# Kernel tuning notes

Measured on AMD Instinct MI355X. Metric: run time of the kernel, lower is better.

## Reference

```python
import jax, jax.numpy as jnp
import numpy as np

EPS = 1.1920929e-07  # torch RMSNorm default eps = finfo(fp32).eps
NUM_HEADS = 8
UP_HEAD = 64
ROPE_HEAD = 32
TOP_K = 4
HIDDEN = 512
INTER = 256
DQ = 256
DKV = 128
N_EXPERTS = 16
B, S = 2, 2048


def _rmsnorm(x, w):
    return x * jax.lax.rsqrt(jnp.mean(x * x, axis=-1, keepdims=True) + EPS) * w


def _rope(x):
    # x: [B, h, S, D] with D = ROPE_HEAD; rotate-half RoPE, base 10000
    D = x.shape[-1]
    s = x.shape[-2]
    inv_freq = 1.0 / (10000.0 ** (jnp.arange(0, D, 2, dtype=jnp.float32) / D))
    freqs = jnp.outer(jnp.arange(s, dtype=jnp.float32), inv_freq)  # [S, D/2]
    emb = jnp.concatenate([freqs, freqs], axis=-1)  # [S, D]
    cos, sin = jnp.cos(emb), jnp.sin(emb)
    x1, x2 = x[..., : D // 2], x[..., D // 2:]
    rot = jnp.concatenate([-x2, x1], axis=-1)
    return x * cos + rot * sin


def _swiglu(x, wg, wu, wd):
    return (jax.nn.silu(x @ wg) * (x @ wu)) @ wd


def setup_inputs() -> dict:
    key = jax.random.key(0)
    ks = jax.random.split(key, 18)
    sd = 0.02
    inp = {
        "hidden_states": jax.random.normal(ks[0], (B, S, HIDDEN), jnp.float32),
        "w_in_norm": jnp.ones((HIDDEN,), jnp.float32),
        "w_dq": sd * jax.random.normal(ks[1], (HIDDEN, DQ), jnp.float32),
        "w_qnorm": jnp.ones((DQ,), jnp.float32),
        "w_uq": sd * jax.random.normal(ks[2], (DQ, NUM_HEADS * (UP_HEAD + ROPE_HEAD)), jnp.float32),
        "w_dkv": sd * jax.random.normal(ks[3], (HIDDEN, DKV + ROPE_HEAD), jnp.float32),
        "w_kvnorm": jnp.ones((DKV,), jnp.float32),
        "w_ukv": sd * jax.random.normal(ks[4], (DKV, NUM_HEADS * UP_HEAD * 2), jnp.float32),
        "w_o": sd * jax.random.normal(ks[5], (NUM_HEADS * UP_HEAD, HIDDEN), jnp.float32),
        "w_post_norm": jnp.ones((HIDDEN,), jnp.float32),
        "w_gate": sd * jax.random.normal(ks[6], (HIDDEN, N_EXPERTS), jnp.float32),
        "sh_wg": sd * jax.random.normal(ks[7], (HIDDEN, INTER), jnp.float32),
        "sh_wu": sd * jax.random.normal(ks[8], (HIDDEN, INTER), jnp.float32),
        "sh_wd": sd * jax.random.normal(ks[9], (INTER, HIDDEN), jnp.float32),
        "r_wg": sd * jax.random.normal(ks[10], (N_EXPERTS, HIDDEN, INTER), jnp.float32),
        "r_wu": sd * jax.random.normal(ks[11], (N_EXPERTS, HIDDEN, INTER), jnp.float32),
        "r_wd": sd * jax.random.normal(ks[12], (N_EXPERTS, INTER, HIDDEN), jnp.float32),
    }
    return inp


def reference(hidden_states, w_in_norm, w_dq, w_qnorm, w_uq, w_dkv, w_kvnorm,
              w_ukv, w_o, w_post_norm, w_gate, sh_wg, sh_wu, sh_wd,
              r_wg, r_wu, r_wd):
    b, s, h = hidden_states.shape
    # ---- MLA attention block ----
    residual = hidden_states
    x = _rmsnorm(hidden_states, w_in_norm)
    c_q = x @ w_dq                                             # [B,S,Dq]
    qcr = _rmsnorm(c_q, w_qnorm) @ w_uq                        # [B,S,nh*(uh+rh)]
    qcr = qcr.reshape(b, s, NUM_HEADS, UP_HEAD + ROPE_HEAD).transpose(0, 2, 1, 3)
    q_c, q_r = qcr[..., :UP_HEAD], qcr[..., UP_HEAD:]
    ckv_kr = x @ w_dkv                                         # [B,S,Dkv+rh]
    c_kv, k_r = ckv_kr[..., :DKV], ckv_kr[..., DKV:]
    k_r = k_r[:, None, :, :]                                   # [B,1,S,rh]
    kv = (_rmsnorm(c_kv, w_kvnorm) @ w_ukv).reshape(b, s, NUM_HEADS, 2 * UP_HEAD).transpose(0, 2, 1, 3)
    k_c, v = kv[..., :UP_HEAD], kv[..., UP_HEAD:]
    q = jnp.concatenate([q_c, _rope(q_r)], axis=-1)            # [B,nh,S,96]
    k = jnp.concatenate([k_c, jnp.broadcast_to(_rope(k_r), (b, NUM_HEADS, s, ROPE_HEAD))], axis=-1)
    scale = 1.0 / jnp.sqrt(jnp.float32(UP_HEAD + ROPE_HEAD))
    attn = jax.nn.softmax(jnp.einsum('bhqd,bhkd->bhqk', q, k) * scale, axis=-1)
    o = jnp.einsum('bhqk,bhkd->bhqd', attn, v).transpose(0, 2, 1, 3).reshape(b, s, NUM_HEADS * UP_HEAD)
    x = o @ w_o + residual
    # ---- MoE block ----
    residual = x
    x = _rmsnorm(x, w_post_norm)
    x2 = x.reshape(-1, h)                                      # [T,H]
    shared = _swiglu(x2, sh_wg, sh_wu, sh_wd)                  # [T,H]
    scores = jax.nn.sigmoid(x2 @ w_gate)                       # [T,E]
    tw, ti = jax.lax.top_k(scores, TOP_K)                      # [T,k]
    tw = tw / jnp.sum(tw, axis=-1, keepdims=True)
    # combine[t,e] = routing weight of expert e for token t (0 if not selected)
    combine = jnp.sum(jax.nn.one_hot(ti, N_EXPERTS, dtype=x2.dtype) * tw[..., None], axis=1)  # [T,E]
    g = jnp.einsum('th,ehi->tei', x2, r_wg)
    u = jnp.einsum('th,ehi->tei', x2, r_wu)
    y = jnp.einsum('tei,eih->teh', jax.nn.silu(g) * u, r_wd)   # per-expert SwiGLU outputs
    routed = jnp.einsum('teh,te->th', y, combine)
    return (shared + routed).reshape(b, s, h) + residual
```

## Files before the change

### kernel.cpp

```cpp
#include <hip/hip_runtime.h>
#include <hip/hip_bf16.h>
#include <math.h>

typedef float f32x4 __attribute__((ext_vector_type(4)));
typedef short s16x8 __attribute__((ext_vector_type(8)));

constexpr int Tt = 4096;
constexpr int NEn = 16;
constexpr float EPSf = 1.1920929e-07f;

__device__ __forceinline__ short f2b(float f) {
    union { __hip_bfloat16 h; short s; } u;
    u.h = __float2bfloat16(f);
    return u.s;
}
__device__ __forceinline__ float b2f(short s) {
    union { float f; unsigned u; } v;
    v.u = ((unsigned)(unsigned short)s) << 16;
    return v.f;
}

constexpr size_t alg(size_t x) { return (x + 15) & ~(size_t)15; }
constexpr size_t OFF_CQKV = 0;
constexpr size_t OFF_QCR  = alg(OFF_CQKV + (size_t)Tt * 416);
constexpr size_t OFF_KVB  = alg(OFF_QCR  + (size_t)Tt * 768);
constexpr size_t OFF_R2   = alg(OFF_KVB  + (size_t)Tt * 1024);
constexpr size_t OFF_TOKE = alg(OFF_R2   + (size_t)Tt * 512);
constexpr size_t OFF_TOKW = alg(OFF_TOKE + (size_t)Tt * 4);
constexpr size_t OFF_EWT  = alg(OFF_TOKW + (size_t)Tt * 4);
constexpr size_t OFF_ECNT = alg(OFF_EWT  + (size_t)NEn * Tt);
constexpr size_t OFF_ETOK = alg(OFF_ECNT + 64);
constexpr size_t OFF_WL   = alg(OFF_ETOK + (size_t)NEn * Tt);
constexpr size_t OFF_WCNT = alg(OFF_WL   + 160);
constexpr size_t OFF_PO   = 0;
constexpr size_t OFF_PL   = (size_t)16 * 2048 * 4 * 64 / 2;
constexpr size_t OFF_XNB   = alg(OFF_WCNT + 16);
constexpr size_t OFF_CQNB  = alg(OFF_XNB   + (size_t)Tt * 512 / 2);
constexpr size_t OFF_CKVNB = alg(OFF_CQNB  + (size_t)Tt * 256 / 2);
constexpr size_t OFF_QB    = alg(OFF_CKVNB + (size_t)Tt * 128 / 2);
constexpr size_t OFF_KB    = alg(OFF_QB    + (size_t)16 * 2048 * 96 / 2);
constexpr size_t OFF_VBT   = alg(OFF_KB    + (size_t)16 * 2048 * 96 / 2);
constexpr size_t OFF_AOB   = alg(OFF_VBT   + (size_t)16 * 64 * 2048 / 2);
constexpr size_t OFF_XN2B  = alg(OFF_AOB   + (size_t)Tt * 512 / 2);
constexpr size_t OFF_GACT  = alg(OFF_XN2B  + (size_t)Tt * 512 / 2);
constexpr size_t OFF_EACT  = alg(OFF_GACT  + (size_t)Tt * 256 / 2);
constexpr size_t OFF_WQKVT = alg(OFF_EACT  + (size_t)16384 * 256 / 2);
constexpr size_t OFF_WUQT  = alg(OFF_WQKVT + (size_t)416 * 512 / 2);
constexpr size_t OFF_WUKVT = alg(OFF_WUQT  + (size_t)768 * 256 / 2);
constexpr size_t OFF_WOT   = alg(OFF_WUKVT + (size_t)1024 * 128 / 2);
constexpr size_t OFF_SHWGT = alg(OFF_WOT   + (size_t)512 * 512 / 2);
constexpr size_t OFF_SHWUT = alg(OFF_SHWGT + (size_t)256 * 512 / 2);
constexpr size_t OFF_SHWDT = alg(OFF_SHWUT + (size_t)256 * 512 / 2);
constexpr size_t OFF_RWGT  = alg(OFF_SHWDT + (size_t)512 * 256 / 2);
constexpr size_t OFF_RWUT  = alg(OFF_RWGT  + (size_t)16 * 256 * 512 / 2);
constexpr size_t OFF_RWDT  = alg(OFF_RWUT  + (size_t)16 * 256 * 512 / 2);

struct CvtTab {
    const float* src[11];
    short* dst[11];
    int K[11], N[11], end[11];
};
__global__ __launch_bounds__(256)
void k_cvt_all(CvtTab tab) {
    __shared__ float t[32][33];
    int bid = blockIdx.x;
    int i = 0;
    while (bid >= tab.end[i]) ++i;
    int tloc = bid - (i ? tab.end[i - 1] : 0);
    int K = tab.K[i], N = tab.N[i];
    int ntiles = N >> 5, perE = ntiles * (K >> 5);
    int e = tloc / perE, rem = tloc - e * perE;
    int k0 = (rem / ntiles) << 5, n0 = (rem % ntiles) << 5;
    size_t eo = (size_t)e * K * N;
    const float* src = tab.src[i];
    short* dst = tab.dst[i];
    int c = threadIdx.x & 31, r = threadIdx.x >> 5;
#pragma unroll
    for (int q = 0; q < 4; ++q)
        t[r + 8 * q][c] = src[eo + (size_t)(k0 + r + 8 * q) * N + n0 + c];
    __syncthreads();
#pragma unroll
    for (int q = 0; q < 4; ++q)
        dst[eo + (size_t)(n0 + r + 8 * q) * K + k0 + c] = f2b(t[c][r + 8 * q]);
}

__global__ void k_rms(const float* __restrict__ in, int inStride, const float* __restrict__ w,
                      short* __restrict__ outB, int outStride, int D) {
    int row = blockIdx.x, tid = threadIdx.x;
    __shared__ float xs[512];
    __shared__ float red[256];
    const float* ip = in + (size_t)row * inStride;
    float ss = 0.f;
    for (int i = tid; i < D; i += 256) { float v = ip[i]; xs[i] = v; ss += v * v; }
    red[tid] = ss; __syncthreads();
    for (int s = 128; s > 0; s >>= 1) { if (tid < s) red[tid] += red[tid + s]; __syncthreads(); }
    float sc = rsqrtf(red[0] / (float)D + EPSf);
    for (int i = tid; i < D; i += 256) outB[(size_t)row * outStride + i] = f2b(xs[i] * sc * w[i]);
}

__global__ void k_rms2(const float* __restrict__ cqkv, const float* __restrict__ wq, short* __restrict__ cqnb,
                       const float* __restrict__ wkv, short* __restrict__ ckvnb) {
    int row = blockIdx.x, tid = threadIdx.x;
    __shared__ float xs[256];
    __shared__ float red[256];
    const float* ip; const float* w; short* ob; int D, outStride, r;
    if (row < Tt) { r = row;      ip = cqkv + (size_t)r * 416;       w = wq;  ob = cqnb;  D = 256; outStride = 256; }
    else          { r = row - Tt; ip = cqkv + (size_t)r * 416 + 256; w = wkv; ob = ckvnb; D = 128; outStride = 128; }
    float ss = 0.f;
    for (int i = tid; i < D; i += 256) { float v = ip[i]; xs[i] = v; ss += v * v; }
    red[tid] = ss; __syncthreads();
    for (int s = 128; s > 0; s >>= 1) { if (tid < s) red[tid] += red[tid + s]; __syncthreads(); }
    float sc = rsqrtf(red[0] / (float)D + EPSf);
    for (int i = tid; i < D; i += 256) ob[(size_t)r * outStride + i] = f2b(xs[i] * sc * w[i]);
}

__global__ __launch_bounds__(256)
void k_rms_router(const float* __restrict__ r2, const float* __restrict__ wpost,
                  const float* __restrict__ wg,
                  short* __restrict__ xn2b, int4* __restrict__ toke, float4* __restrict__ tokw) {
    int t = blockIdx.x, tid = threadIdx.x;
    __shared__ float xs[512];
    __shared__ float red[256];
    __shared__ float part[16][17];
    __shared__ float sc[16];
    const float* ip = r2 + (size_t)t * 512;
    float ss = 0.f;
    for (int i = tid; i < 512; i += 256) { float v = ip[i]; xs[i] = v; ss += v * v; }
    red[tid] = ss; __syncthreads();
    for (int s = 128; s > 0; s >>= 1) { if (tid < s) red[tid] += red[tid + s]; __syncthreads(); }
    float scale = rsqrtf(red[0] / 512.f + EPSf);
    for (int i = tid; i < 512; i += 256) {
        float v = xs[i] * scale * wpost[i];
        xs[i] = v;
        xn2b[(size_t)t * 512 + i] = f2b(v);
    }
    __syncthreads();
    {
        int e = tid & 15, ch = tid >> 4;
        const float* wp = wg + (size_t)ch * 32 * 16 + e;
        float s = 0.f;
#pragma unroll 8
        for (int k = 0; k < 32; ++k) s = fmaf(xs[ch * 32 + k], wp[(size_t)k * 16], s);
        part[ch][e] = s;
    }
    __syncthreads();
    if (tid < 16) {
        float s = 0.f;
#pragma unroll
        for (int c = 0; c < 16; ++c) s += part[c][tid];
        sc[tid] = 1.f / (1.f + expf(-s));
    }
    __syncthreads();
    if (tid < 64) {
        int lane = tid, e = lane & 15;
        float scv = sc[e];
        unsigned sel = 0;
        float tw[4]; int ti[4];
#pragma unroll
        for (int kk = 0; kk < 4; ++kk) {
            float cand = ((sel >> e) & 1u) ? -1e30f : scv;
            float mx = cand;
            mx = fmaxf(mx, __shfl_xor(mx, 1));
            mx = fmaxf(mx, __shfl_xor(mx, 2));
            mx = fmaxf(mx, __shfl_xor(mx, 4));
            mx = fmaxf(mx, __shfl_xor(mx, 8));
            unsigned long long msk = __ballot(cand == mx);
            int bi = (__ffsll(msk) - 1) & 15;
            tw[kk] = mx; ti[kk] = bi;
            sel |= 1u << bi;
        }
        if (lane == 0) {
            float inv = 1.f / (tw[0] + tw[1] + tw[2] + tw[3]);
            toke[t] = make_int4(ti[0], ti[1], ti[2], ti[3]);
            tokw[t] = make_float4(tw[0] * inv, tw[1] * inv, tw[2] * inv, tw[3] * inv);
        }
    }
}

template <int EPI>
__global__ __launch_bounds__(512)
void k_mgemm(const short* __restrict__ A, const short* __restrict__ BT,
             float* __restrict__ C, const float* __restrict__ add, int N, int K) {
    __shared__ __align__(16) short As[64 * 64];
    __shared__ __align__(16) short Bs[64 * 64];
    int tid = threadIdx.x;
    int w = tid >> 6, l = tid & 63, g = l >> 4, li = l & 15;
    int wm = w >> 1, wn = w & 1;
    int m0 = blockIdx.y * 64, n0 = blockIdx.x * 64;
    f32x4 acc[2] = {};
    for (int k0 = 0; k0 < K; k0 += 64) {
        __syncthreads();
        {
            int row = tid >> 3, ch = tid & 7;
            *(int4*)&As[row * 64 + ((ch ^ (row & 7)) * 8)] =
                *(const int4*)(A + (size_t)(m0 + row) * K + k0 + 8 * ch);
            int4 v = {0, 0, 0, 0};
            if (n0 + row < N) v = *(const int4*)(BT + (size_t)(n0 + row) * K + k0 + 8 * ch);
            *(int4*)&Bs[row * 64 + ((ch ^ (row & 7)) * 8)] = v;
        }
        __syncthreads();
#pragma unroll
        for (int kc = 0; kc < 2; ++kc) {
            int row = wm * 16 + li;
            s16x8 af = *(const s16x8*)&As[row * 64 + (((4 * kc + g) ^ (li & 7)) * 8)];
#pragma unroll
            for (int nt = 0; nt < 2; ++nt) {
                int n = wn * 32 + nt * 16 + li;
                s16x8 bf = *(const s16x8*)&Bs[n * 64 + (((4 * kc + g) ^ (li & 7)) * 8)];
                acc[nt] = __builtin_amdgcn_mfma_f32_16x16x32_bf16(af, bf, acc[nt], 0, 0, 0);
            }
        }
    }
#pragma unroll
    for (int nt = 0; nt < 2; ++nt)
#pragma unroll
        for (int r = 0; r < 4; ++r) {
            int gm = m0 + wm * 16 + 4 * g + r;
            int gn = n0 + wn * 32 + nt * 16 + li;
            if (gn < N) {
                float v = acc[nt][r];
                if (EPI == 1) v += add[(size_t)gm * N + gn];
                C[(size_t)gm * N + gn] = v;
            }
        }
}

__global__ __launch_bounds__(512)
void k_shexp(const short* __restrict__ X, const short* __restrict__ WGt, const short* __restrict__ WUt,
             short* __restrict__ gact) {
    __shared__ __align__(16) short As[64 * 64];
    __shared__ __align__(16) short Bg[64 * 64];
    __shared__ __align__(16) short Bu[64 * 64];
    int tid = threadIdx.x;
    int w = tid >> 6, l = tid & 63, g = l >> 4, li = l & 15;
    int wm = w >> 1, wn = w & 1;
    int m0 = blockIdx.x * 64, n0 = blockIdx.y * 64;
    f32x4 ag[2] = {}, au[2] = {};
    for (int k0 = 0; k0 < 512; k0 += 64) {
        __syncthreads();
        {
            int row = tid >> 3, ch = tid & 7;
            *(int4*)&As[row * 64 + ((ch ^ (row & 7)) * 8)] =
                *(const int4*)(X + (size_t)(m0 + row) * 512 + k0 + 8 * ch);
            *(int4*)&Bg[row * 64 + ((ch ^ (row & 7)) * 8)] =
                *(const int4*)(WGt + (size_t)(n0 + row) * 512 + k0 + 8 * ch);
            *(int4*)&Bu[row * 64 + ((ch ^ (row & 7)) * 8)] =
                *(const int4*)(WUt + (size_t)(n0 + row) * 512 + k0 + 8 * ch);
        }
        __syncthreads();
#pragma unroll
        for (int kc = 0; kc < 2; ++kc) {
            int row = wm * 16 + li;
            s16x8 af = *(const s16x8*)&As[row * 64 + (((4 * kc + g) ^ (li & 7)) * 8)];
#pragma unroll
            for (int nt = 0; nt < 2; ++nt) {
                int n = wn * 32 + nt * 16 + li;
                s16x8 bg = *(const s16x8*)&Bg[n * 64 + (((4 * kc + g) ^ (li & 7)) * 8)];
                s16x8 bu = *(const s16x8*)&Bu[n * 64 + (((4 * kc + g) ^ (li & 7)) * 8)];
                ag[nt] = __builtin_amdgcn_mfma_f32_16x16x32_bf16(af, bg, ag[nt], 0, 0, 0);
                au[nt] = __builtin_amdgcn_mfma_f32_16x16x32_bf16(af, bu, au[nt], 0, 0, 0);
            }
        }
    }
#pragma unroll
    for (int nt = 0; nt < 2; ++nt)
#pragma unroll
        for (int r = 0; r < 4; ++r) {
            int gm = m0 + wm * 16 + 4 * g + r;
            int gn = n0 + wn * 32 + nt * 16 + li;
            float gv = ag[nt][r], uv = au[nt][r];
            gact[(size_t)gm * 256 + gn] = f2b(gv / (1.f + __expf(-gv)) * uv);
        }
}

__global__ void k_build_qkv(const float* __restrict__ qcr, const float* __restrict__ kvb,
                            const float* __restrict__ cqkv,
                            short* __restrict__ qb, short* __restrict__ kb, short* __restrict__ vbt) {
    const float scale = 0.14724389f;
    int gid = blockIdx.x * 256 + threadIdx.x;
    const int NQ = 16 * 2048 * 96;
    if (gid < NQ) {
        int d = gid % 96;
        int rs = gid / 96;
        int srow = rs & 2047;
        int bh = rs >> 11;
        int b = bh >> 3, h = bh & 7;
        int t = b * 2048 + srow;
        const float* src = qcr + (size_t)t * 768 + h * 96;
        float val;
        if (d < 64) {
            val = src[d];
        } else {
            int d2 = d - 64;
            int fi = d2 & 15;
            float ang = (float)srow * __expf(-((float)(2 * fi) / 32.f) * 9.210340371976184f);
            float s, c; __sincosf(ang, &s, &c);
            float x = src[64 + d2];
            float r = (d2 < 16) ? -src[64 + d2 + 16] : src[64 + d2 - 16];
            val = x * c + r * s;
        }
        qb[gid] = f2b(val * scale);
    } else if (gid < 2 * NQ) {
        int g2 = gid - NQ;
        int d = g2 % 96;
        int rs = g2 / 96;
        int srow = rs & 2047;
        int bh = rs >> 11;
        int b = bh >> 3, h = bh & 7;
        int t = b * 2048 + srow;
        float val;
        if (d < 64) {
            val = kvb[(size_t)t * 1024 + h * 128 + d];
        } else {
            int d2 = d - 64;
            int fi = d2 & 15;
            float ang = (float)srow * __expf(-((float)(2 * fi) / 32.f) * 9.210340371976184f);
            float s, c; __sincosf(ang, &s, &c);
            float x = cqkv[(size_t)t * 416 + 384 + d2];
            float r = (d2 < 16) ? -cqkv[(size_t)t * 416 + 384 + d2 + 16]
                                :  cqkv[(size_t)t * 416 + 384 + d2 - 16];
            val = x * c + r * s;
        }
        kb[g2] = f2b(val);
    } else {
        int g2 = gid - 2 * NQ;
        int key = g2 & 2047;
        int dim = (g2 >> 11) & 63;
        int bh = g2 >> 17;
        int b = bh >> 3, h = bh & 7;
        vbt[g2] = f2b(kvb[(size_t)(b * 2048 + key) * 1024 + h * 128 + 64 + dim]);
    }
}

__global__ __launch_bounds__(256)
void k_attn(const short* __restrict__ qb, const short* __restrict__ kb,
            const short* __restrict__ vbt, short* __restrict__ po, float* __restrict__ pl) {
    __shared__ __align__(16) short Ks[64 * 100];
    __shared__ __align__(16) short Vs[80 * 64];
    int tid = threadIdx.x;
    int w = tid >> 6, l = tid & 63, g = l >> 4, li = l & 15;
    int blk = blockIdx.x;
    int bh = blk >> 6, rem = blk & 63;
    int qt = rem >> 2, ks = rem & 3;
    int qc0 = qt * 128 + w * 32;

    {
        const short one = 0x3F80;
        for (int i = tid; i < 16 * 64; i += 256)
            Vs[64 * 64 + i] = (i < 64) ? one : (short)0;
    }

    s16x8 qf[2][3];
#pragma unroll
    for (int j = 0; j < 2; ++j) {
        const short* qp = qb + (size_t)(bh * 2048 + qc0 + j * 16 + li) * 96;
#pragma unroll
        for (int c = 0; c < 3; ++c) qf[j][c] = *(const s16x8*)(qp + 32 * c + 8 * g);
    }

    f32x4 o[2][5] = {};
    const short* kbase = kb + (size_t)bh * 2048 * 96;
    const short* vbase = vbt + (size_t)bh * 64 * 2048;

    for (int t = 0; t < 8; ++t) {
        int koff = ks * 512 + t * 64;
        __syncthreads();
#pragma unroll
        for (int p = 0; p < 3; ++p) {
            int flat = p * 256 + tid;
            int key = flat / 12, u = flat % 12;
            *(int4*)&Ks[key * 100 + 8 * u] = *(const int4*)(kbase + (size_t)(koff + key) * 96 + 8 * u);
        }
#pragma unroll
        for (int p = 0; p < 2; ++p) {
            int flat = p * 256 + tid;
            int dim = flat >> 3, kc8 = flat & 7;
            int4 v = *(const int4*)(vbase + (size_t)dim * 2048 + koff + 8 * kc8);
            int sw = dim & 15;
            *(int2*)&Vs[dim * 64 + (((2 * kc8) ^ sw) * 4)]     = make_int2(v.x, v.y);
            *(int2*)&Vs[dim * 64 + (((2 * kc8 + 1) ^ sw) * 4)] = make_int2(v.z, v.w);
        }
        __syncthreads();

        f32x4 s[2][4];
#pragma unroll
        for (int kt = 0; kt < 4; ++kt) {
            f32x4 a0 = {}, a1 = {};
#pragma unroll
            for (int c = 0; c < 3; ++c) {
                s16x8 kf = *(const s16x8*)&Ks[(kt * 16 + li) * 100 + 32 * c + 8 * g];
                a0 = __builtin_amdgcn_mfma_f32_16x16x32_bf16(kf, qf[0][c], a0, 0, 0, 0);
                a1 = __builtin_amdgcn_mfma_f32_16x16x32_bf16(kf, qf[1][c], a1, 0, 0, 0);
            }
            s[0][kt] = a0; s[1][kt] = a1;
        }
#pragma unroll
        for (int j = 0; j < 2; ++j)
#pragma unroll
            for (int kt = 0; kt < 4; ++kt)
#pragma unroll
                for (int r = 0; r < 4; ++r) s[j][kt][r] = exp2f(s[j][kt][r]);
        s16x8 pf[2][2];
#pragma unroll
        for (int j = 0; j < 2; ++j)
#pragma unroll
            for (int kc = 0; kc < 2; ++kc) {
                s16x8 tt;
#pragma unroll
                for (int r = 0; r < 4; ++r) { tt[r] = f2b(s[j][2 * kc][r]); tt[4 + r] = f2b(s[j][2 * kc + 1][r]); }
                pf[j][kc] = tt;
            }
#pragma unroll
        for (int dt = 0; dt < 5; ++dt) {
            int dim = dt * 16 + li;
#pragma unroll
            for (int kc = 0; kc < 2; ++kc) {
                int2 a0 = *(const int2*)&Vs[dim * 64 + (((8 * kc + g) ^ li) * 4)];
                int2 a1 = *(const int2*)&Vs[dim * 64 + (((8 * kc + 4 + g) ^ li) * 4)];
                union { s16x8 v; int i[4]; } vf;
                vf.i[0] = a0.x; vf.i[1] = a0.y; vf.i[2] = a1.x; vf.i[3] = a1.y;
                o[0][dt] = __builtin_amdgcn_mfma_f32_16x16x32_bf16(vf.v, pf[0][kc], o[0][dt], 0, 0, 0);
                o[1][dt] = __builtin_amdgcn_mfma_f32_16x16x32_bf16(vf.v, pf[1][kc], o[1][dt], 0, 0, 0);
            }
        }
    }
#pragma unroll
    for (int j = 0; j < 2; ++j) {
        int qcol = qc0 + j * 16 + li;
        size_t qbase = ((size_t)(bh * 2048 + qcol) * 4 + ks) * 64;
#pragma unroll
        for (int dt = 0; dt < 4; ++dt)
#pragma unroll
            for (int r = 0; r < 4; ++r)
                po[qbase + dt * 16 + 4 * g + r] = f2b(o[j][dt][r]);
        if (g == 0) pl[(size_t)(bh * 2048 + qcol) * 4 + ks] = o[j][4][0];
    }
}

__global__ __launch_bounds__(256)
void k_attn_comb(const short* __restrict__ po, const float* __restrict__ pl, short* __restrict__ ao) {
    int gid = blockIdx.x * 256 + threadIdx.x;
    int d = gid & 63;
    int q = (gid >> 6) & 2047;
    int bh = gid >> 17;
    int b = bh >> 3, h = bh & 7;
    size_t pb = ((size_t)(bh * 2048 + q) * 4) * 64 + d;
    float os = 0.f;
#pragma unroll
    for (int ks = 0; ks < 4; ++ks) os += b2f(po[pb + 64 * ks]);
    size_t lb = (size_t)(bh * 2048 + q) * 4;
    float ls = pl[lb] + pl[lb + 1] + pl[lb + 2] + pl[lb + 3];
    ao[(size_t)(b * 2048 + q) * 512 + h * 64 + d] = f2b(os / ls);
}

__global__ __launch_bounds__(256)
void k_scatter(const int4* __restrict__ toke, const float4* __restrict__ tokw,
               float* __restrict__ ewt, int* __restrict__ ecnt, int* __restrict__ etok) {
    __shared__ int lcnt[16];
    __shared__ int lbase[16];
    int tid = threadIdx.x;
    int t = blockIdx.x * 256 + tid;
    if (tid < 16) lcnt[tid] = 0;
    __syncthreads();
    int4 e4 = toke[t];
    float4 w4 = tokw[t];
    int es[4] = { e4.x, e4.y, e4.z, e4.w };
    float wv[4] = { w4.x, w4.y, w4.z, w4.w };
    int ls[4];
#pragma unroll
    for (int kk = 0; kk < 4; ++kk) ls[kk] = atomicAdd(&lcnt[es[kk]], 1);
    __syncthreads();
    if (tid < 16) lbase[tid] = atomicAdd(&ecnt[tid], lcnt[tid]);
    __syncthreads();
#pragma unroll
    for (int kk = 0; kk < 4; ++kk) {
        int slot = lbase[es[kk]] + ls[kk];
        etok[es[kk] * 4096 + slot] = t * 4 + kk;
        ewt[es[kk] * 4096 + slot] = wv[kk];
    }
}

__global__ void k_worklist(const int* __restrict__ ecnt, int* __restrict__ wl, int* __restrict__ wcnt) {
    if (threadIdx.x == 0 && blockIdx.x == 0) {
        int c = 0;
        for (int e = 0; e < 16; ++e) {
            int n = (ecnt[e] + 127) >> 7;
            for (int i = 0; i < n; ++i) wl[c++] = (e << 20) | (i << 7);
        }
        wcnt[0] = c;
    }
}

__global__ __launch_bounds__(512)
void k_moe1m(const short* __restrict__ X, const short* __restrict__ WGt, const short* __restrict__ WUt,
             const int* __restrict__ ecnt, const int* __restrict__ etok,
             const int* __restrict__ wl, const int* __restrict__ wcnt,
             short* __restrict__ eact) {
    if ((int)blockIdx.x >= wcnt[0]) return;
    int ent = wl[blockIdx.x];
    int e = ent >> 20, base = ent & 0xFFFFF;
    int rows = min(128, ecnt[e] - base);
    int n0 = blockIdx.y * 64;
    __shared__ __align__(16) short As[128 * 64];
    __shared__ __align__(16) short Bg[64 * 64];
    __shared__ __align__(16) short Bu[64 * 64];
    __shared__ int toks[128];
    int tid = threadIdx.x;
    if (tid < 128) toks[tid] = (tid < rows) ? etok[e * 4096 + base + tid] : -1;
    __syncthreads();
    int w = tid >> 6, l = tid & 63, g = l >> 4, li = l & 15;
    int wm = w >> 1, wn = w & 1;
    const short* wgp = WGt + (size_t)e * 256 * 512;
    const short* wup = WUt + (size_t)e * 256 * 512;
    f32x4 ag[2][2] = {}, au[2][2] = {};
    for (int k0 = 0; k0 < 512; k0 += 64) {
        __syncthreads();
#pragma unroll
        for (int p = 0; p < 2; ++p) {
            int flat = p * 512 + tid;
            int row = flat >> 3, ch = flat & 7;
            int tk = toks[row];
            int4 v = {0, 0, 0, 0};
            if (tk >= 0) v = *(const int4*)(X + (size_t)(tk >> 2) * 512 + k0 + 8 * ch);
            *(int4*)&As[row * 64 + ((ch ^ (row & 7)) * 8)] = v;
        }
        {
            int n = tid >> 3, ch = tid & 7;
            *(int4*)&Bg[n * 64 + ((ch ^ (n & 7)) * 8)] = *(const int4*)(wgp + (size_t)(n0 + n) * 512 + k0 + 8 * ch);
            *(int4*)&Bu[n * 64 + ((ch ^ (n & 7)) * 8)] = *(const int4*)(wup + (size_t)(n0 + n) * 512 + k0 + 8 * ch);
        }
        __syncthreads();
#pragma unroll
        for (int kc = 0; kc < 2; ++kc) {
            s16x8 af[2], bg[2], bu[2];
#pragma unroll
            for (int mt = 0; mt < 2; ++mt) {
                int row = wm * 32 + mt * 16 + li;
                af[mt] = *(const s16x8*)&As[row * 64 + (((4 * kc + g) ^ (li & 7)) * 8)];
            }
#pragma unroll
            for (int nt = 0; nt < 2; ++nt) {
                int n = wn * 32 + nt * 16 + li;
                bg[nt] = *(const s16x8*)&Bg[n * 64 + (((4 * kc + g) ^ (li & 7)) * 8)];
                bu[nt] = *(const s16x8*)&Bu[n * 64 + (((4 * kc + g) ^ (li & 7)) * 8)];
            }
#pragma unroll
            for (int mt = 0; mt < 2; ++mt)
#pragma unroll
                for (int nt = 0; nt < 2; ++nt) {
                    ag[mt][nt] = __builtin_amdgcn_mfma_f32_16x16x32_bf16(af[mt], bg[nt], ag[mt][nt], 0, 0, 0);
                    au[mt][nt] = __builtin_amdgcn_mfma_f32_16x16x32_bf16(af[mt], bu[nt], au[mt][nt], 0, 0, 0);
                }
        }
    }
#pragma unroll
    for (int mt = 0; mt < 2; ++mt)
#pragma unroll
        for (int nt = 0; nt < 2; ++nt)
#pragma unroll
            for (int r = 0; r < 4; ++r) {
                int local = wm * 32 + mt * 16 + 4 * g + r;
                if (local < rows) {
                    int entry = toks[local];
                    int gn = n0 + wn * 32 + nt * 16 + li;
                    float gv = ag[mt][nt][r], uv = au[mt][nt][r];
                    eact[(size_t)entry * 256 + gn] = f2b(gv / (1.f + __expf(-gv)) * uv);
                }
            }
}

__global__ __launch_bounds__(512)
void k_moe2m(const short* __restrict__ EA, const short* __restrict__ WDt,
             const int* __restrict__ ecnt, const int* __restrict__ etok,
             const int* __restrict__ wl, const int* __restrict__ wcnt,
             const float* __restrict__ ewt, float* __restrict__ oacc) {
    if ((int)blockIdx.x >= wcnt[0]) return;
    int ent = wl[blockIdx.x];
    int e = ent >> 20, base = ent & 0xFFFFF;
    int rows = min(128, ecnt[e] - base);
    int n0 = blockIdx.y * 64;
    __shared__ __align__(16) short As[128 * 64];
    __shared__ __align__(16) short Bs[64 * 64];
    __shared__ int toks[128];
    __shared__ float wts[128];
    int tid = threadIdx.x;
    if (tid < 128) {
        toks[tid] = (tid < rows) ? etok[e * 4096 + base + tid] : -1;
        wts[tid]  = (tid < rows) ? ewt[e * 4096 + base + tid] : 0.f;
    }
    __syncthreads();
    int w = tid >> 6, l = tid & 63, g = l >> 4, li = l & 15;
    int wm = w >> 1, wn = w & 1;
    const short* wdp = WDt + (size_t)e * 512 * 256;
    f32x4 acc[2][2] = {};
    for (int k0 = 0; k0 < 256; k0 += 64) {
        __syncthreads();
#pragma unroll
        for (int p = 0; p < 2; ++p) {
            int flat = p * 512 + tid;
            int row = flat >> 3, ch = flat & 7;
            int tk = toks[row];
            int4 v = {0, 0, 0, 0};
            if (tk >= 0) v = *(const int4*)(EA + (size_t)tk * 256 + k0 + 8 * ch);
            *(int4*)&As[row * 64 + ((ch ^ (row & 7)) * 8)] = v;
        }
        {
            int n = tid >> 3, ch = tid & 7;
            *(int4*)&Bs[n * 64 + ((ch ^ (n & 7)) * 8)] = *(const int4*)(wdp + (size_t)(n0 + n) * 256 + k0 + 8 * ch);
        }
        __syncthreads();
#pragma unroll
        for (int kc = 0; kc < 2; ++kc) {
            s16x8 af[2], bf[2];
#pragma unroll
            for (int mt = 0; mt < 2; ++mt) {
                int row = wm * 32 + mt * 16 + li;
                af[mt] = *(const s16x8*)&As[row * 64 + (((4 * kc + g) ^ (li & 7)) * 8)];
            }
#pragma unroll
            for (int nt = 0; nt < 2; ++nt) {
                int n = wn * 32 + nt * 16 + li;
                bf[nt] = *(const s16x8*)&Bs[n * 64 + (((4 * kc + g) ^ (li & 7)) * 8)];
            }
#pragma unroll
            for (int mt = 0; mt < 2; ++mt)
#pragma unroll
                for (int nt = 0; nt < 2; ++nt)
                    acc[mt][nt] = __builtin_amdgcn_mfma_f32_16x16x32_bf16(af[mt], bf[nt], acc[mt][nt], 0, 0, 0);
        }
    }
#pragma unroll
    for (int mt = 0; mt < 2; ++mt)
#pragma unroll
        for (int nt = 0; nt < 2; ++nt)
#pragma unroll
            for (int r = 0; r < 4; ++r) {
                int local = wm * 32 + mt * 16 + 4 * g + r;
                if (local < rows) {
                    int tok = toks[local] >> 2;
                    int gn = n0 + wn * 32 + nt * 16 + li;
                    atomicAdd(&oacc[(size_t)tok * 512 + gn], acc[mt][nt][r] * wts[local]);
                }
            }
}

extern "C" void kernel_launch(void* const* d_in, const int* in_sizes, int n_in,
                              void* d_out, int out_size, void* d_ws, size_t ws_size,
                              hipStream_t stream) {
    const float* hs       = (const float*)d_in[0];
    const float* w_innorm = (const float*)d_in[1];
    const float* w_dq     = (const float*)d_in[2];
    const float* w_qnorm  = (const float*)d_in[3];
    const float* w_uq     = (const float*)d_in[4];
    const float* w_dkv    = (const float*)d_in[5];
    const float* w_kvnorm = (const float*)d_in[6];
    const float* w_ukv    = (const float*)d_in[7];
    const float* w_o      = (const float*)d_in[8];
    const float* w_post   = (const float*)d_in[9];
    const float* w_gate   = (const float*)d_in[10];
    const float* sh_wg    = (const float*)d_in[11];
    const float* sh_wu    = (const float*)d_in[12];
    const float* sh_wd    = (const float*)d_in[13];
    const float* r_wg     = (const float*)d_in[14];
    const float* r_wu     = (const float*)d_in[15];
    const float* r_wd     = (const float*)d_in[16];

    float* ws   = (float*)d_ws;
    float* cqkv = ws + OFF_CQKV;
    float* qcr  = ws + OFF_QCR;
    float* kvb  = ws + OFF_KVB;
    float* r2   = ws + OFF_R2;
    short* po   = (short*)(ws + OFF_PO);
    float* pl   = ws + OFF_PL;
    int4*  toke = (int4*)(ws + OFF_TOKE);
    float4* tokw = (float4*)(ws + OFF_TOKW);
    float* ewt  = ws + OFF_EWT;
    int*   ecnt = (int*)(ws + OFF_ECNT);
    int*   etok = (int*)(ws + OFF_ETOK);
    int*   wl   = (int*)(ws + OFF_WL);
    int*   wcnt = (int*)(ws + OFF_WCNT);
    short* xnb   = (short*)(ws + OFF_XNB);
    short* cqnb  = (short*)(ws + OFF_CQNB);
    short* ckvnb = (short*)(ws + OFF_CKVNB);
    short* qb    = (short*)(ws + OFF_QB);
    short* kb    = (short*)(ws + OFF_KB);
    short* vbt   = (short*)(ws + OFF_VBT);
    short* aob   = (short*)(ws + OFF_AOB);
    short* xn2b  = (short*)(ws + OFF_XN2B);
    short* gact  = (short*)(ws + OFF_GACT);
    short* eact  = (short*)(ws + OFF_EACT);
    short* wqkvT = (short*)(ws + OFF_WQKVT);
    short* wuqT  = (short*)(ws + OFF_WUQT);
    short* wukvT = (short*)(ws + OFF_WUKVT);
    short* woT   = (short*)(ws + OFF_WOT);
    short* shwgT = (short*)(ws + OFF_SHWGT);
    short* shwuT = (short*)(ws + OFF_SHWUT);
    short* shwdT = (short*)(ws + OFF_SHWDT);
    short* rwgT  = (short*)(ws + OFF_RWGT);
    short* rwuT  = (short*)(ws + OFF_RWUT);
    short* rwdT  = (short*)(ws + OFF_RWDT);

    float* outF = (float*)d_out;

    CvtTab tab;
    const float* srcs[11] = { w_dq, w_dkv, w_uq, w_ukv, w_o, sh_wg, sh_wu, sh_wd, r_wg, r_wu, r_wd };
    short* dsts[11] = { wqkvT, wqkvT + (size_t)256 * 512, wuqT, wukvT, woT, shwgT, shwuT, shwdT, rwgT, rwuT, rwdT };
    int Ks_[11] = { 512, 512, 256, 128, 512, 512, 512, 256, 512, 512, 256 };
    int Ns_[11] = { 256, 160, 768, 1024, 512, 256, 256, 512, 256, 256, 512 };
    int Es_[11] = { 1, 1, 1, 1, 1, 1, 1, 1, 16, 16, 16 };
    int cum = 0;
    for (int i = 0; i < 11; ++i) {
        tab.src[i] = srcs[i]; tab.dst[i] = dsts[i];
        tab.K[i] = Ks_[i]; tab.N[i] = Ns_[i];
        cum += Es_[i] * (Ks_[i] >> 5) * (Ns_[i] >> 5);
        tab.end[i] = cum;
    }
    k_cvt_all<<<cum, 256, 0, stream>>>(tab);

    k_rms<<<Tt, 256, 0, stream>>>(hs, 512, w_innorm, xnb, 512, 512);
    k_mgemm<0><<<dim3(7, 64), 512, 0, stream>>>(xnb, wqkvT, cqkv, nullptr, 416, 512);
    k_rms2<<<2 * Tt, 256, 0, stream>>>(cqkv, w_qnorm, cqnb, w_kvnorm, ckvnb);
    k_mgemm<0><<<dim3(12, 64), 512, 0, stream>>>(cqnb, wuqT, qcr, nullptr, 768, 256);
    k_mgemm<0><<<dim3(16, 64), 512, 0, stream>>>(ckvnb, wukvT, kvb, nullptr, 1024, 128);
    k_build_qkv<<<(2 * 16 * 2048 * 96 + 16 * 64 * 2048) / 256, 256, 0, stream>>>(qcr, kvb, cqkv, qb, kb, vbt);
    k_attn<<<1024, 256, 0, stream>>>(qb, kb, vbt, po, pl);
    k_attn_comb<<<(16 * 2048 * 64) / 256, 256, 0, stream>>>(po, pl, aob);
    k_mgemm<1><<<dim3(8, 64), 512, 0, stream>>>(aob, woT, r2, hs, 512, 512);
    k_rms_router<<<Tt, 256, 0, stream>>>(r2, w_post, w_gate, xn2b, toke, tokw);
    k_shexp<<<dim3(64, 4), 512, 0, stream>>>(xn2b, shwgT, shwuT, gact);
    k_mgemm<1><<<dim3(8, 64), 512, 0, stream>>>(gact, shwdT, outF, r2, 512, 256);
    hipMemsetAsync(ecnt, 0, NEn * sizeof(int), stream);
    k_scatter<<<16, 256, 0, stream>>>(toke, tokw, ewt, ecnt, etok);
    k_worklist<<<1, 64, 0, stream>>>(ecnt, wl, wcnt);
    k_moe1m<<<dim3(144, 4), 512, 0, stream>>>(xn2b, rwgT, rwuT, ecnt, etok, wl, wcnt, eact);
    k_moe2m<<<dim3(144, 8), 512, 0, stream>>>(eact, rwdT, ecnt, etok, wl, wcnt, ewt, outF);
}
```

Baseline: 240.8 us.

## Fuse attention combine into Wo GEMM, emit bf16 up-projections, drop worklist kernel

Three separate changes. The split-K attention partials are now reduced and normalised inside the Wo projection GEMM's A-tile load, which removes the separate combine kernel and its bf16 intermediate buffer. The q/kv up-projection GEMMs write bf16 instead of fp32, halving that traffic into the QKV build kernel. The single-thread worklist kernel is removed, and each MoE block finds its expert/tile from the counts in shared memory. The costs are a small extra loop per MoE block and redundant partial reduction across the N-tile blocks of the Wo GEMM.

Measured after the change: 229.1 us. 1.05x faster.

```diff
diff --git a/kernel.cpp b/kernel.cpp
--- a/kernel.cpp
+++ b/kernel.cpp
@@ -30,18 +30,15 @@
 constexpr size_t OFF_EWT  = alg(OFF_TOKW + (size_t)Tt * 4);
 constexpr size_t OFF_ECNT = alg(OFF_EWT  + (size_t)NEn * Tt);
 constexpr size_t OFF_ETOK = alg(OFF_ECNT + 64);
-constexpr size_t OFF_WL   = alg(OFF_ETOK + (size_t)NEn * Tt);
-constexpr size_t OFF_WCNT = alg(OFF_WL   + 160);
 constexpr size_t OFF_PO   = 0;
 constexpr size_t OFF_PL   = (size_t)16 * 2048 * 4 * 64 / 2;
-constexpr size_t OFF_XNB   = alg(OFF_WCNT + 16);
+constexpr size_t OFF_XNB   = alg(OFF_ETOK + (size_t)NEn * Tt);
 constexpr size_t OFF_CQNB  = alg(OFF_XNB   + (size_t)Tt * 512 / 2);
 constexpr size_t OFF_CKVNB = alg(OFF_CQNB  + (size_t)Tt * 256 / 2);
 constexpr size_t OFF_QB    = alg(OFF_CKVNB + (size_t)Tt * 128 / 2);
 constexpr size_t OFF_KB    = alg(OFF_QB    + (size_t)16 * 2048 * 96 / 2);
 constexpr size_t OFF_VBT   = alg(OFF_KB    + (size_t)16 * 2048 * 96 / 2);
-constexpr size_t OFF_AOB   = alg(OFF_VBT   + (size_t)16 * 64 * 2048 / 2);
-constexpr size_t OFF_XN2B  = alg(OFF_AOB   + (size_t)Tt * 512 / 2);
+constexpr size_t OFF_XN2B  = alg(OFF_VBT   + (size_t)16 * 64 * 2048 / 2);
 constexpr size_t OFF_GACT  = alg(OFF_XN2B  + (size_t)Tt * 512 / 2);
 constexpr size_t OFF_EACT  = alg(OFF_GACT  + (size_t)Tt * 256 / 2);
 constexpr size_t OFF_WQKVT = alg(OFF_EACT  + (size_t)16384 * 256 / 2);
@@ -180,7 +177,7 @@
 template <int EPI>
 __global__ __launch_bounds__(512)
 void k_mgemm(const short* __restrict__ A, const short* __restrict__ BT,
-             float* __restrict__ C, const float* __restrict__ add, int N, int K) {
+             void* __restrict__ Cv, const float* __restrict__ add, int N, int K) {
     __shared__ __align__(16) short As[64 * 64];
     __shared__ __align__(16) short Bs[64 * 64];
     int tid = threadIdx.x;
@@ -220,8 +217,67 @@
             if (gn < N) {
                 float v = acc[nt][r];
                 if (EPI == 1) v += add[(size_t)gm * N + gn];
-                C[(size_t)gm * N + gn] = v;
-            }
+                if (EPI == 2) ((short*)Cv)[(size_t)gm * N + gn] = f2b(v);
+                else          ((float*)Cv)[(size_t)gm * N + gn] = v;
+            }
+        }
+}
+
+__global__ __launch_bounds__(512)
+void k_wo_gemm(const short* __restrict__ po, const float* __restrict__ pl,
+               const short* __restrict__ BT, float* __restrict__ C,
+               const float* __restrict__ add) {
+    constexpr int N = 512, K = 512;
+    __shared__ __align__(16) short As[64 * 64];
+    __shared__ __align__(16) short Bs[64 * 64];
+    int tid = threadIdx.x;
+    int w = tid >> 6, l = tid & 63, g = l >> 4, li = l & 15;
+    int wm = w >> 1, wn = w & 1;
+    int m0 = blockIdx.y * 64, n0 = blockIdx.x * 64;
+    int row = tid >> 3, ch = tid & 7;
+    int t = m0 + row;
+    int b = t >> 11, q = t & 2047;
+    f32x4 acc[2] = {};
+    for (int k0 = 0; k0 < K; k0 += 64) {
+        int h = k0 >> 6;
+        int bhq = (b * 8 + h) * 2048 + q;
+        size_t pb = (size_t)bhq * 256 + 8 * ch;
+        float4 l4 = *(const float4*)(pl + (size_t)bhq * 4);
+        float inv = 1.f / (l4.x + l4.y + l4.z + l4.w);
+        union { int4 v; short s[8]; } p0, p1, p2, p3, ov;
+        p0.v = *(const int4*)(po + pb);
+        p1.v = *(const int4*)(po + pb + 64);
+        p2.v = *(const int4*)(po + pb + 128);
+        p3.v = *(const int4*)(po + pb + 192);
+#pragma unroll
+        for (int i = 0; i < 8; ++i) {
+            float os = b2f(p0.s[i]) + b2f(p1.s[i]) + b2f(p2.s[i]) + b2f(p3.s[i]);
+            ov.s[i] = f2b(os * inv);
+        }
+        int4 bv = *(const int4*)(BT + (size_t)(n0 + row) * K + k0 + 8 * ch);
+        __syncthreads();
+        *(int4*)&As[row * 64 + ((ch ^ (row & 7)) * 8)] = ov.v;
+        *(int4*)&Bs[row * 64 + ((ch ^ (row & 7)) * 8)] = bv;
+        __syncthreads();
+#pragma unroll
+        for (int kc = 0; kc < 2; ++kc) {
+            int rr = wm * 16 + li;
+            s16x8 af = *(const s16x8*)&As[rr * 64 + (((4 * kc + g) ^ (li & 7)) * 8)];
+#pragma unroll
+            for (int nt = 0; nt < 2; ++nt) {
+                int n = wn * 32 + nt * 16 + li;
+                s16x8 bf = *(const s16x8*)&Bs[n * 64 + (((4 * kc + g) ^ (li & 7)) * 8)];
+                acc[nt] = __builtin_amdgcn_mfma_f32_16x16x32_bf16(af, bf, acc[nt], 0, 0, 0);
+            }
+        }
+    }
+#pragma unroll
+    for (int nt = 0; nt < 2; ++nt)
+#pragma unroll
+        for (int r = 0; r < 4; ++r) {
+            int gm = m0 + wm * 16 + 4 * g + r;
+            int gn = n0 + wn * 32 + nt * 16 + li;
+            C[(size_t)gm * N + gn] = acc[nt][r] + add[(size_t)gm * N + gn];
         }
 }
 
@@ -273,7 +329,7 @@
         }
 }
 
-__global__ void k_build_qkv(const float* __restrict__ qcr, const float* __restrict__ kvb,
+__global__ void k_build_qkv(const short* __restrict__ qcrb, const short* __restrict__ kvbb,
                             const float* __restrict__ cqkv,
                             short* __restrict__ qb, short* __restrict__ kb, short* __restrict__ vbt) {
     const float scale = 0.14724389f;
@@ -286,17 +342,17 @@
         int bh = rs >> 11;
         int b = bh >> 3, h = bh & 7;
         int t = b * 2048 + srow;
-        const float* src = qcr + (size_t)t * 768 + h * 96;
+        const short* src = qcrb + (size_t)t * 768 + h * 96;
         float val;
         if (d < 64) {
-            val = src[d];
+            val = b2f(src[d]);
         } else {
             int d2 = d - 64;
             int fi = d2 & 15;
             float ang = (float)srow * __expf(-((float)(2 * fi) / 32.f) * 9.210340371976184f);
             float s, c; __sincosf(ang, &s, &c);
-            float x = src[64 + d2];
-            float r = (d2 < 16) ? -src[64 + d2 + 16] : src[64 + d2 - 16];
+            float x = b2f(src[64 + d2]);
+            float r = (d2 < 16) ? -b2f(src[64 + d2 + 16]) : b2f(src[64 + d2 - 16]);
             val = x * c + r * s;
         }
         qb[gid] = f2b(val * scale);
@@ -308,9 +364,8 @@
         int bh = rs >> 11;
         int b = bh >> 3, h = bh & 7;
         int t = b * 2048 + srow;
-        float val;
         if (d < 64) {
-            val = kvb[(size_t)t * 1024 + h * 128 + d];
+            kb[g2] = kvbb[(size_t)t * 1024 + h * 128 + d];
         } else {
             int d2 = d - 64;
             int fi = d2 & 15;
@@ -319,16 +374,15 @@
             float x = cqkv[(size_t)t * 416 + 384 + d2];
             float r = (d2 < 16) ? -cqkv[(size_t)t * 416 + 384 + d2 + 16]
                                 :  cqkv[(size_t)t * 416 + 384 + d2 - 16];
-            val = x * c + r * s;
-        }
-        kb[g2] = f2b(val);
+            kb[g2] = f2b(x * c + r * s);
+        }
     } else {
         int g2 = gid - 2 * NQ;
         int key = g2 & 2047;
         int dim = (g2 >> 11) & 63;
         int bh = g2 >> 17;
         int b = bh >> 3, h = bh & 7;
-        vbt[g2] = f2b(kvb[(size_t)(b * 2048 + key) * 1024 + h * 128 + 64 + dim]);
+        vbt[g2] = kvbb[(size_t)(b * 2048 + key) * 1024 + h * 128 + 64 + dim];
     }
 }
 
@@ -438,22 +492,6 @@
 }
 
 __global__ __launch_bounds__(256)
-void k_attn_comb(const short* __restrict__ po, const float* __restrict__ pl, short* __restrict__ ao) {
-    int gid = blockIdx.x * 256 + threadIdx.x;
-    int d = gid & 63;
-    int q = (gid >> 6) & 2047;
-    int bh = gid >> 17;
-    int b = bh >> 3, h = bh & 7;
-    size_t pb = ((size_t)(bh * 2048 + q) * 4) * 64 + d;
-    float os = 0.f;
-#pragma unroll
-    for (int ks = 0; ks < 4; ++ks) os += b2f(po[pb + 64 * ks]);
-    size_t lb = (size_t)(bh * 2048 + q) * 4;
-    float ls = pl[lb] + pl[lb + 1] + pl[lb + 2] + pl[lb + 3];
-    ao[(size_t)(b * 2048 + q) * 512 + h * 64 + d] = f2b(os / ls);
-}
-
-__global__ __launch_bounds__(256)
 void k_scatter(const int4* __restrict__ toke, const float4* __restrict__ tokw,
                float* __restrict__ ewt, int* __restrict__ ecnt, int* __restrict__ etok) {
     __shared__ int lcnt[16];
@@ -480,32 +518,23 @@
     }
 }
 
-__global__ void k_worklist(const int* __restrict__ ecnt, int* __restrict__ wl, int* __restrict__ wcnt) {
-    if (threadIdx.x == 0 && blockIdx.x == 0) {
-        int c = 0;
-        for (int e = 0; e < 16; ++e) {
-            int n = (ecnt[e] + 127) >> 7;
-            for (int i = 0; i < n; ++i) wl[c++] = (e << 20) | (i << 7);
-        }
-        wcnt[0] = c;
-    }
-}
-
 __global__ __launch_bounds__(512)
 void k_moe1m(const short* __restrict__ X, const short* __restrict__ WGt, const short* __restrict__ WUt,
-             const int* __restrict__ ecnt, const int* __restrict__ etok,
-             const int* __restrict__ wl, const int* __restrict__ wcnt,
-             short* __restrict__ eact) {
-    if ((int)blockIdx.x >= wcnt[0]) return;
-    int ent = wl[blockIdx.x];
-    int e = ent >> 20, base = ent & 0xFFFFF;
-    int rows = min(128, ecnt[e] - base);
-    int n0 = blockIdx.y * 64;
+             const int* __restrict__ ecnt, const int* __restrict__ etok, short* __restrict__ eact) {
+    __shared__ int ecs[16];
     __shared__ __align__(16) short As[128 * 64];
     __shared__ __align__(16) short Bg[64 * 64];
     __shared__ __align__(16) short Bu[64 * 64];
     __shared__ int toks[128];
     int tid = threadIdx.x;
+    if (tid < 16) ecs[tid] = ecnt[tid];
+    __syncthreads();
+    int bid = blockIdx.x, e = 0;
+    for (; e < 16; ++e) { int n = (ecs[e] + 127) >> 7; if (bid < n) break; bid -= n; }
+    if (e >= 16) return;
+    int base = bid << 7;
+    int rows = min(128, ecs[e] - base);
+    int n0 = blockIdx.y * 64;
     if (tid < 128) toks[tid] = (tid < rows) ? etok[e * 4096 + base + tid] : -1;
     __syncthreads();
     int w = tid >> 6, l = tid & 63, g = l >> 4, li = l & 15;
@@ -572,18 +601,21 @@
 __global__ __launch_bounds__(512)
 void k_moe2m(const short* __restrict__ EA, const short* __restrict__ WDt,
              const int* __restrict__ ecnt, const int* __restrict__ etok,
-             const int* __restrict__ wl, const int* __restrict__ wcnt,
              const float* __restrict__ ewt, float* __restrict__ oacc) {
-    if ((int)blockIdx.x >= wcnt[0]) return;
-    int ent = wl[blockIdx.x];
-    int e = ent >> 20, base = ent & 0xFFFFF;
-    int rows = min(128, ecnt[e] - base);
-    int n0 = blockIdx.y * 64;
+    __shared__ int ecs[16];
     __shared__ __align__(16) short As[128 * 64];
     __shared__ __align__(16) short Bs[64 * 64];
     __shared__ int toks[128];
     __shared__ float wts[128];
     int tid = threadIdx.x;
+    if (tid < 16) ecs[tid] = ecnt[tid];
+    __syncthreads();
+    int bid = blockIdx.x, e = 0;
+    for (; e < 16; ++e) { int n = (ecs[e] + 127) >> 7; if (bid < n) break; bid -= n; }
+    if (e >= 16) return;
+    int base = bid << 7;
+    int rows = min(128, ecs[e] - base);
+    int n0 = blockIdx.y * 64;
     if (tid < 128) {
         toks[tid] = (tid < rows) ? etok[e * 4096 + base + tid] : -1;
         wts[tid]  = (tid < rows) ? ewt[e * 4096 + base + tid] : 0.f;
@@ -667,8 +699,8 @@
 
     float* ws   = (float*)d_ws;
     float* cqkv = ws + OFF_CQKV;
-    float* qcr  = ws + OFF_QCR;
-    float* kvb  = ws + OFF_KVB;
+    short* qcrb = (short*)(ws + OFF_QCR);
+    short* kvbb = (short*)(ws + OFF_KVB);
     float* r2   = ws + OFF_R2;
     short* po   = (short*)(ws + OFF_PO);
     float* pl   = ws + OFF_PL;
@@ -677,15 +709,12 @@
     float* ewt  = ws + OFF_EWT;
     int*   ecnt = (int*)(ws + OFF_ECNT);
     int*   etok = (int*)(ws + OFF_ETOK);
-    int*   wl   = (int*)(ws + OFF_WL);
-    int*   wcnt = (int*)(ws + OFF_WCNT);
     short* xnb   = (short*)(ws + OFF_XNB);
     short* cqnb  = (short*)(ws + OFF_CQNB);
     short* ckvnb = (short*)(ws + OFF_CKVNB);
     short* qb    = (short*)(ws + OFF_QB);
     short* kb    = (short*)(ws + OFF_KB);
     short* vbt   = (short*)(ws + OFF_VBT);
-    short* aob   = (short*)(ws + OFF_AOB);
     short* xn2b  = (short*)(ws + OFF_XN2B);
     short* gact  = (short*)(ws + OFF_GACT);
     short* eact  = (short*)(ws + OFF_EACT);
@@ -718,20 +747,18 @@
     k_cvt_all<<<cum, 256, 0, stream>>>(tab);
 
     k_rms<<<Tt, 256, 0, stream>>>(hs, 512, w_innorm, xnb, 512, 512);
-    k_mgemm<0><<<dim3(7, 64), 512, 0, stream>>>(xnb, wqkvT, cqkv, nullptr, 416, 512);
+    k_mgemm<0><<<dim3(7, 64), 512, 0, stream>>>(xnb, wqkvT, (void*)cqkv, nullptr, 416, 512);
     k_rms2<<<2 * Tt, 256, 0, stream>>>(cqkv, w_qnorm, cqnb, w_kvnorm, ckvnb);
-    k_mgemm<0><<<dim3(12, 64), 512, 0, stream>>>(cqnb, wuqT, qcr, nullptr, 768, 256);
-    k_mgemm<0><<<dim3(16, 64), 512, 0, stream>>>(ckvnb, wukvT, kvb, nullptr, 1024, 128);
-    k_build_qkv<<<(2 * 16 * 2048 * 96 + 16 * 64 * 2048) / 256, 256, 0, stream>>>(qcr, kvb, cqkv, qb, kb, vbt);
+    k_mgemm<2><<<dim3(12, 64), 512, 0, stream>>>(cqnb, wuqT, (void*)qcrb, nullptr, 768, 256);
+    k_mgemm<2><<<dim3(16, 64), 512, 0, stream>>>(ckvnb, wukvT, (void*)kvbb, nullptr, 1024, 128);
+    k_build_qkv<<<(2 * 16 * 2048 * 96 + 16 * 64 * 2048) / 256, 256, 0, stream>>>(qcrb, kvbb, cqkv, qb, kb, vbt);
     k_attn<<<1024, 256, 0, stream>>>(qb, kb, vbt, po, pl);
-    k_attn_comb<<<(16 * 2048 * 64) / 256, 256, 0, stream>>>(po, pl, aob);
-    k_mgemm<1><<<dim3(8, 64), 512, 0, stream>>>(aob, woT, r2, hs, 512, 512);
+    k_wo_gemm<<<dim3(8, 64), 512, 0, stream>>>(po, pl, woT, r2, hs);
     k_rms_router<<<Tt, 256, 0, stream>>>(r2, w_post, w_gate, xn2b, toke, tokw);
     k_shexp<<<dim3(64, 4), 512, 0, stream>>>(xn2b, shwgT, shwuT, gact);
-    k_mgemm<1><<<dim3(8, 64), 512, 0, stream>>>(gact, shwdT, outF, r2, 512, 256);
+    k_mgemm<1><<<dim3(8, 64), 512, 0, stream>>>(gact, shwdT, (void*)outF, r2, 512, 256);
     hipMemsetAsync(ecnt, 0, NEn * sizeof(int), stream);
     k_scatter<<<16, 256, 0, stream>>>(toke, tokw, ewt, ecnt, etok);
-    k_worklist<<<1, 64, 0, stream>>>(ecnt, wl, wcnt);
-    k_moe1m<<<dim3(144, 4), 512, 0, stream>>>(xn2b, rwgT, rwuT, ecnt, etok, wl, wcnt, eact);
-    k_moe2m<<<dim3(144, 8), 512, 0, stream>>>(eact, rwdT, ecnt, etok, wl, wcnt, ewt, outF);
-}
+    k_moe1m<<<dim3(144, 4), 512, 0, stream>>>(xn2b, rwgT, rwuT, ecnt, etok, eact);
+    k_moe2m<<<dim3(144, 8), 512, 0, stream>>>(eact, rwdT, ecnt, etok, ewt, outF);
+}
```
